# Performance work log

Measured on AMD Instinct MI355X. Metric: run time of the kernel, lower is better.

## Reference

```python
import jax, jax.numpy as jnp
import numpy as np

N = 100000
E = 1600000
IN = 256
H = 4
F = 64
NEG_SLOPE = 0.05


def setup_inputs() -> dict:
    key = jax.random.key(0)
    ks = jax.random.split(key, 8)
    feat = jax.random.normal(ks[0], (N, IN), dtype=jnp.float32)
    src = jax.random.randint(ks[1], (E,), 0, N, dtype=jnp.int64)
    dst = jax.random.randint(ks[2], (E,), 0, N, dtype=jnp.int64)
    W_fc = jax.random.normal(ks[3], (H * F, IN), dtype=jnp.float32) * (2.0 / np.sqrt(IN + H * F))
    attn_l = jax.random.normal(ks[4], (H, F), dtype=jnp.float32) * 0.1
    attn_r = jax.random.normal(ks[5], (H, F), dtype=jnp.float32) * 0.1
    W_res = jax.random.normal(ks[6], (H * F, IN), dtype=jnp.float32) * (2.0 / np.sqrt(IN + H * F))
    bias = jnp.zeros((H * F,), dtype=jnp.float32)
    return {"feat": feat, "src": src, "dst": dst, "W_fc": W_fc,
            "attn_l": attn_l, "attn_r": attn_r, "W_res": W_res, "bias": bias}


def _leaky_relu(x):
    return jnp.where(x > 0, x, NEG_SLOPE * x)


def reference(feat, src, dst, W_fc, attn_l, attn_r, W_res, bias):
    # project: [N, H, F]
    feat_src = (feat @ W_fc.T).reshape(N, H, F)
    # attention logits per node: el/er [N, H]
    el = jnp.einsum('nhf,hf->nh', feat_src, attn_l)
    er = jnp.einsum('nhf,hf->nh', feat_src, attn_r)
    # edge SDDMM (u_add_v) + leaky_relu: [E, H]
    e = _leaky_relu(el[src] + er[dst])
    # edge softmax grouped by destination node
    emax = jax.ops.segment_max(e, dst, num_segments=N)          # [N, H]
    emax = jnp.where(jnp.isfinite(emax), emax, 0.0)             # empty segments
    ex = jnp.exp(e - emax[dst])                                 # [E, H]
    esum = jax.ops.segment_sum(ex, dst, num_segments=N)         # [N, H]
    a = ex / jnp.maximum(esum[dst], 1e-20)                      # [E, H]
    # u_mul_e + sum aggregation (SpMM): [N, H, F]
    msgs = feat_src[src] * a[:, :, None]                        # [E, H, F]
    rst = jax.ops.segment_sum(msgs, dst, num_segments=N)
    # residual + bias
    rst = rst + (feat @ W_res.T).reshape(N, H, F)
    rst = rst + bias.reshape(1, H, F)
    return rst, a
```

## Files before the change

### kernel.cpp

```cpp
#include <hip/hip_runtime.h>

#define NNODES 100000
#define NEDGES 1600000
#define KDIM 256
#define CDIM 256
#define NHEAD 4
#define FDIM 64
#define NEG 0.05f

typedef short bf16x8 __attribute__((ext_vector_type(8)));
typedef float f32x4  __attribute__((ext_vector_type(4)));
typedef __attribute__((address_space(3))) void*       lds_vp;
typedef __attribute__((address_space(1))) const void* glb_cvp;

__device__ __forceinline__ unsigned short f2b(float x) {
    unsigned int u = __float_as_uint(x);
    return (unsigned short)((u + 0x7FFFu + ((u >> 16) & 1u)) >> 16);
}
__device__ __forceinline__ float b2f(unsigned short b) {
    return __uint_as_float(((unsigned int)b) << 16);
}
__device__ __forceinline__ float lrelu(float x) { return x > 0.f ? x : NEG * x; }

__device__ __forceinline__ unsigned int fmap(float f) {
    unsigned int u = __float_as_uint(f);
    return u ^ ((u >> 31) ? 0xFFFFFFFFu : 0x80000000u);
}
__device__ __forceinline__ float funmap(unsigned int u) {
    return __uint_as_float(u ^ ((u & 0x80000000u) ? 0x80000000u : 0xFFFFFFFFu));
}

__global__ __launch_bounds__(256) void cvt_feat(const float* __restrict__ in,
                                                unsigned short* __restrict__ out)
{
    int i = (blockIdx.x * 256 + threadIdx.x) * 4;
    float4 v = *(const float4*)(in + i);
    ushort4 o;
    o.x = f2b(v.x); o.y = f2b(v.y); o.z = f2b(v.z); o.w = f2b(v.w);
    *(ushort4*)(out + i) = o;
}

__global__ __launch_bounds__(256) void cvt_w(const float* __restrict__ Wfc,
                                             const float* __restrict__ Wres,
                                             unsigned short* __restrict__ out)
{
    int i = (blockIdx.x * 256 + threadIdx.x) * 4;
    float4 v = (i < 65536) ? *(const float4*)(Wfc + i)
                           : *(const float4*)(Wres + (i - 65536));
    ushort4 o;
    o.x = f2b(v.x); o.y = f2b(v.y); o.z = f2b(v.z); o.w = f2b(v.w);
    *(ushort4*)(out + i) = o;
}

__global__ __launch_bounds__(256) void gemm_mfma(
    const unsigned short* __restrict__ featb,
    const unsigned short* __restrict__ Wb,
    const float* __restrict__ bias,
    const float* __restrict__ attn_l, const float* __restrict__ attn_r,
    unsigned short* __restrict__ fsb,
    float* __restrict__ rst,
    float* __restrict__ el, float* __restrict__ er)
{
    const int b = blockIdx.x;
    const int grp = b >> 5, w32 = b & 31;
    const int bx = grp * 8 + (w32 & 7);
    const int ny = w32 >> 3;
    if (bx >= (NNODES + 127) / 128) return;

    __shared__ __align__(16) char smem[32768];
    char* sA = smem;
    char* sB = smem + 16384;

    const int tid = threadIdx.x;
    const int w = tid >> 6, l = tid & 63;
    const int wm = w & 1, wn = w >> 1;
    const int row0 = bx * 128;

    f32x4 acc[4][4];
#pragma unroll
    for (int tm = 0; tm < 4; ++tm)
#pragma unroll
        for (int tn = 0; tn < 4; ++tn) acc[tm][tn] = (f32x4)0.f;

    const int srow = tid >> 3;
    const int sslot = tid & 7;

    for (int k0 = 0; k0 < 256; k0 += 64) {
        if (k0) __syncthreads();
#pragma unroll
        for (int it = 0; it < 4; ++it) {
            int r = srow + it * 32;
            int gr = row0 + r; if (gr >= NNODES) gr = NNODES - 1;
            int kc = sslot ^ (r & 7);
            const unsigned short* g = featb + (size_t)gr * 256 + k0 + kc * 8;
            void* sp = sA + (it * 256 + w * 64) * 16;
            __builtin_amdgcn_global_load_lds((glb_cvp)g, (lds_vp)sp, 16, 0, 0);
        }
#pragma unroll
        for (int it = 0; it < 4; ++it) {
            int r = srow + it * 32;
            int kc = sslot ^ (r & 7);
            const unsigned short* g = Wb + (size_t)(ny * 128 + r) * 256 + k0 + kc * 8;
            void* sp = sB + (it * 256 + w * 64) * 16;
            __builtin_amdgcn_global_load_lds((glb_cvp)g, (lds_vp)sp, 16, 0, 0);
        }
        __syncthreads();

        const int quad = l >> 4;
#pragma unroll
        for (int kk = 0; kk < 2; ++kk) {
            const int kc = kk * 4 + quad;
            bf16x8 af[4], bq[4];
#pragma unroll
            for (int tm = 0; tm < 4; ++tm) {
                int m = wm * 64 + tm * 16 + (l & 15);
                af[tm] = *(const bf16x8*)(sA + m * 128 + ((kc ^ (m & 7)) * 16));
            }
#pragma unroll
            for (int tn = 0; tn < 4; ++tn) {
                int n = wn * 64 + tn * 16 + (l & 15);
                bq[tn] = *(const bf16x8*)(sB + n * 128 + ((kc ^ (n & 7)) * 16));
            }
#pragma unroll
            for (int tm = 0; tm < 4; ++tm)
#pragma unroll
                for (int tn = 0; tn < 4; ++tn)
                    acc[tm][tn] = __builtin_amdgcn_mfma_f32_16x16x32_bf16(
                        af[tm], bq[tn], acc[tm][tn], 0, 0, 0);
        }
    }

    const int quad = l >> 4, c15 = l & 15;
    if (ny < 2) {
#pragma unroll
        for (int tm = 0; tm < 4; ++tm) {
            int rb = row0 + wm * 64 + tm * 16 + quad * 4;
#pragma unroll
            for (int tn = 0; tn < 4; ++tn) {
                int cg = ny * 128 + wn * 64 + tn * 16 + c15;
#pragma unroll
                for (int reg = 0; reg < 4; ++reg) {
                    int r = rb + reg;
                    if (r < NNODES) fsb[(size_t)r * 256 + cg] = f2b(acc[tm][tn][reg]);
                }
            }
        }
        const int hh = ny * 2 + wn;
        float alv[4], arv[4];
#pragma unroll
        for (int tn = 0; tn < 4; ++tn) {
            alv[tn] = attn_l[hh * 64 + tn * 16 + c15];
            arv[tn] = attn_r[hh * 64 + tn * 16 + c15];
        }
#pragma unroll
        for (int tm = 0; tm < 4; ++tm) {
#pragma unroll
            for (int reg = 0; reg < 4; ++reg) {
                float pl = 0.f, pr = 0.f;
#pragma unroll
                for (int tn = 0; tn < 4; ++tn) {
                    float v = acc[tm][tn][reg];
                    pl = fmaf(v, alv[tn], pl);
                    pr = fmaf(v, arv[tn], pr);
                }
#pragma unroll
                for (int d = 1; d < 16; d <<= 1) {
                    pl += __shfl_xor(pl, d);
                    pr += __shfl_xor(pr, d);
                }
                if (c15 == 0) {
                    int r = row0 + wm * 64 + tm * 16 + quad * 4 + reg;
                    if (r < NNODES) {
                        el[r * NHEAD + hh] = pl;
                        er[r * NHEAD + hh] = pr;
                    }
                }
            }
        }
    } else {
#pragma unroll
        for (int tm = 0; tm < 4; ++tm) {
            int rb = row0 + wm * 64 + tm * 16 + quad * 4;
#pragma unroll
            for (int tn = 0; tn < 4; ++tn) {
                int co = (ny - 2) * 128 + wn * 64 + tn * 16 + c15;
                float b2 = bias[co];
#pragma unroll
                for (int reg = 0; reg < 4; ++reg) {
                    int r = rb + reg;
                    if (r < NNODES) rst[(size_t)r * 256 + co] = acc[tm][tn][reg] + b2;
                }
            }
        }
    }
}

__global__ __launch_bounds__(256) void gmax_kernel(const float* __restrict__ el,
                                                   unsigned int* __restrict__ gmax)
{
    int t = blockIdx.x * 256 + threadIdx.x;
    float4 mx = make_float4(-1e30f, -1e30f, -1e30f, -1e30f);
    for (int n = t; n < NNODES; n += 64 * 256) {
        float4 v = *(const float4*)(el + (size_t)n * 4);
        mx.x = fmaxf(mx.x, v.x); mx.y = fmaxf(mx.y, v.y);
        mx.z = fmaxf(mx.z, v.z); mx.w = fmaxf(mx.w, v.w);
    }
#pragma unroll
    for (int d = 32; d > 0; d >>= 1) {
        mx.x = fmaxf(mx.x, __shfl_xor(mx.x, d));
        mx.y = fmaxf(mx.y, __shfl_xor(mx.y, d));
        mx.z = fmaxf(mx.z, __shfl_xor(mx.z, d));
        mx.w = fmaxf(mx.w, __shfl_xor(mx.w, d));
    }
    if ((threadIdx.x & 63) == 0) {
        atomicMax(&gmax[0], fmap(mx.x));
        atomicMax(&gmax[1], fmap(mx.y));
        atomicMax(&gmax[2], fmap(mx.z));
        atomicMax(&gmax[3], fmap(mx.w));
    }
}

__global__ __launch_bounds__(256) void count_kernel(const int* __restrict__ dst,
                                                    int* __restrict__ cnt)
{
    int e = blockIdx.x * 256 + threadIdx.x;
    if (e < NEDGES) atomicAdd(&cnt[dst[e]], 1);
}

__global__ __launch_bounds__(256) void offset_kernel(const int* __restrict__ cnt,
                                                     int* __restrict__ off,
                                                     int* __restrict__ cursor,
                                                     int* __restrict__ total)
{
    int n = blockIdx.x * 256 + threadIdx.x;
    int lane = threadIdx.x & 63;
    int c = (n < NNODES) ? cnt[n] : 0;
    int incl = c;
#pragma unroll
    for (int d = 1; d < 64; d <<= 1) {
        int t = __shfl_up(incl, d);
        if (lane >= d) incl += t;
    }
    int wsum = __shfl(incl, 63);
    int base = 0;
    if (lane == 0) base = atomicAdd(total, wsum);
    base = __shfl(base, 0);
    if (n < NNODES) {
        int o = base + incl - c;
        off[n] = o;
        cursor[n] = o;
    }
}

__global__ __launch_bounds__(256) void scatter_kernel(const int* __restrict__ dst,
                                                      int* __restrict__ cursor,
                                                      int* __restrict__ perm)
{
    int e = blockIdx.x * 256 + threadIdx.x;
    if (e < NEDGES) {
        int p = atomicAdd(&cursor[dst[e]], 1);
        perm[p] = e;
    }
}

__global__ __launch_bounds__(256) void agg_kernel(
    const int* __restrict__ src, const int* __restrict__ perm,
    const int* __restrict__ off, const int* __restrict__ cnt,
    const float* __restrict__ el, const float* __restrict__ er,
    const unsigned int* __restrict__ gmax,
    const unsigned short* __restrict__ fsb,
    float* __restrict__ rst,
    float* __restrict__ a_out)
{
    const int tid = threadIdx.x;
    const int wv = tid >> 6, lane = tid & 63;
    const int n = blockIdx.x * 4 + wv;
    const int deg = cnt[n];
    if (deg == 0) return;
    const int o0 = off[n];

    __shared__ __align__(16) float a_sh[4][64][4];
    float* aw = &a_sh[wv][0][0];

    const float4 er4 = *(const float4*)(er + (size_t)n * NHEAD);
    const uint4 g4 = *(const uint4*)gmax;
    float4 M;
    M.x = lrelu(funmap(g4.x) + er4.x);
    M.y = lrelu(funmap(g4.y) + er4.y);
    M.z = lrelu(funmap(g4.z) + er4.z);
    M.w = lrelu(funmap(g4.w) + er4.w);

    float4 s = make_float4(0.f, 0.f, 0.f, 0.f);
    int s0_save = 0, e0_save = 0;
    float4 l0_save = make_float4(0.f, 0.f, 0.f, 0.f);

    for (int base = 0; base < deg; base += 64) {
        int i = base + lane;
        bool valid = i < deg;
        int e = perm[o0 + (valid ? i : deg - 1)];
        int sidx = src[e];
        float4 ev = *(const float4*)(el + (size_t)sidx * NHEAD);
        float4 l;
        l.x = lrelu(ev.x + er4.x); l.y = lrelu(ev.y + er4.y);
        l.z = lrelu(ev.z + er4.z); l.w = lrelu(ev.w + er4.w);
        if (base == 0) { s0_save = sidx; e0_save = e; l0_save = l; }
        s.x += valid ? __expf(l.x - M.x) : 0.f;
        s.y += valid ? __expf(l.y - M.y) : 0.f;
        s.z += valid ? __expf(l.z - M.z) : 0.f;
        s.w += valid ? __expf(l.w - M.w) : 0.f;
    }
#pragma unroll
    for (int d = 32; d > 0; d >>= 1) {
        s.x += __shfl_xor(s.x, d);
        s.y += __shfl_xor(s.y, d);
        s.z += __shfl_xor(s.z, d);
        s.w += __shfl_xor(s.w, d);
    }
    float4 inv;
    inv.x = 1.f / fmaxf(s.x, 1e-20f);
    inv.y = 1.f / fmaxf(s.y, 1e-20f);
    inv.z = 1.f / fmaxf(s.z, 1e-20f);
    inv.w = 1.f / fmaxf(s.w, 1e-20f);

    const int rsel = lane >> 5;
    const int c    = lane & 31;
    const int h2   = c >> 3;
    const unsigned int coff = (unsigned)c << 4;

    float acc[8];
#pragma unroll
    for (int k = 0; k < 8; ++k) acc[k] = 0.f;

    for (int base = 0; base < deg; base += 64) {
        int i = base + lane;
        bool valid = i < deg;
        int sidx, e; float4 l;
        if (base == 0) { sidx = s0_save; e = e0_save; l = l0_save; }
        else {
            e = perm[o0 + (valid ? i : deg - 1)];
            sidx = src[e];
            float4 ev = *(const float4*)(el + (size_t)sidx * NHEAD);
            l.x = lrelu(ev.x + er4.x); l.y = lrelu(ev.y + er4.y);
            l.z = lrelu(ev.z + er4.z); l.w = lrelu(ev.w + er4.w);
        }
        float4 a;
        a.x = valid ? __expf(l.x - M.x) * inv.x : 0.f;
        a.y = valid ? __expf(l.y - M.y) * inv.y : 0.f;
        a.z = valid ? __expf(l.z - M.z) * inv.z : 0.f;
        a.w = valid ? __expf(l.w - M.w) * inv.w : 0.f;
        *(float4*)(aw + (lane << 2)) = a;

        if (valid) *(float4*)(a_out + (size_t)e * NHEAD) = a;

        int nc = min(64, deg - base);
#pragma unroll 4
        for (int jj = 0; jj < nc; jj += 2) {
            int sjA = __builtin_amdgcn_readlane(sidx, jj);
            int sjB = __builtin_amdgcn_readlane(sidx, jj + 1);
            float av = aw[((jj + rsel) << 2) + h2];
            int sj = rsel ? sjB : sjA;
            unsigned int boff = ((unsigned)sj << 9) + coff;
            uint4 p = *(const uint4*)((const char*)fsb + boff);
            acc[0] = fmaf(av, __uint_as_float(p.x << 16),         acc[0]);
            acc[1] = fmaf(av, __uint_as_float(p.x & 0xffff0000u), acc[1]);
            acc[2] = fmaf(av, __uint_as_float(p.y << 16),         acc[2]);
            acc[3] = fmaf(av, __uint_as_float(p.y & 0xffff0000u), acc[3]);
            acc[4] = fmaf(av, __uint_as_float(p.z << 16),         acc[4]);
            acc[5] = fmaf(av, __uint_as_float(p.z & 0xffff0000u), acc[5]);
            acc[6] = fmaf(av, __uint_as_float(p.w << 16),         acc[6]);
            acc[7] = fmaf(av, __uint_as_float(p.w & 0xffff0000u), acc[7]);
        }
    }
#pragma unroll
    for (int k = 0; k < 8; ++k) acc[k] += __shfl_xor(acc[k], 32);
    float o0v = rsel ? acc[4] : acc[0];
    float o1v = rsel ? acc[5] : acc[1];
    float o2v = rsel ? acc[6] : acc[2];
    float o3v = rsel ? acc[7] : acc[3];
    size_t ro = (size_t)n * 256 + ((size_t)c << 3) + ((size_t)rsel << 2);
    float4 r = *(float4*)(rst + ro);
    r.x += o0v; r.y += o1v; r.z += o2v; r.w += o3v;
    *(float4*)(rst + ro) = r;
}

extern "C" void kernel_launch(void* const* d_in, const int* in_sizes, int n_in,
                              void* d_out, int out_size, void* d_ws, size_t ws_size,
                              hipStream_t stream) {
    const float* feat   = (const float*)d_in[0];
    const int*   src    = (const int*)d_in[1];
    const int*   dst    = (const int*)d_in[2];
    const float* Wfc    = (const float*)d_in[3];
    const float* attn_l = (const float*)d_in[4];
    const float* attn_r = (const float*)d_in[5];
    const float* Wres   = (const float*)d_in[6];
    const float* bias   = (const float*)d_in[7];

    float* rst   = (float*)d_out;
    float* a_out = (float*)d_out + (size_t)NNODES * CDIM;

    unsigned short* featb = (unsigned short*)d_ws;
    unsigned short* fsb   = featb + (size_t)NNODES * CDIM;
    unsigned short* Wb    = fsb + (size_t)NNODES * CDIM;
    float* el      = (float*)(Wb + 512 * 256);
    float* er      = el + (size_t)NNODES * NHEAD;
    unsigned int* gmax = (unsigned int*)(er + (size_t)NNODES * NHEAD);
    int* cnt    = (int*)(gmax + 4);
    int* off    = cnt + NNODES;
    int* cursor = off + NNODES;
    int* total  = cursor + NNODES;
    int* perm   = total + 4;

    hipMemsetAsync(cnt, 0, NNODES * sizeof(int), stream);
    hipMemsetAsync(total, 0, 4 * sizeof(int), stream);
    hipMemsetAsync(gmax, 0, 4 * sizeof(unsigned int), stream);

    cvt_feat<<<(NNODES * CDIM) / (256 * 4), 256, 0, stream>>>(feat, featb);
    cvt_w<<<(512 * 256) / (256 * 4), 256, 0, stream>>>(Wfc, Wres, Wb);

    gemm_mfma<<<3136, 256, 0, stream>>>(featb, Wb, bias, attn_l, attn_r,
                                        fsb, rst, el, er);

    gmax_kernel<<<64, 256, 0, stream>>>(el, gmax);

    count_kernel<<<(NEDGES + 255) / 256, 256, 0, stream>>>(dst, cnt);
    offset_kernel<<<(NNODES + 255) / 256, 256, 0, stream>>>(cnt, off, cursor, total);
    scatter_kernel<<<(NEDGES + 255) / 256, 256, 0, stream>>>(dst, cursor, perm);

    agg_kernel<<<NNODES / 4, 256, 0, stream>>>(src, perm, off, cnt, el, er, gmax,
                                               fsb, rst, a_out);
}
```

Measured before the change: 691.6 us.

## Fuse degree count into feature convert and pack src with edge permutation

The destination degree count moves into the bf16 feature-conversion kernel, removing one launch. The scatter step now writes (edge, src) pairs into a buffer that reuses the bf16 feature workspace, which is dead after the GEMM. This removes the dependent src[e] gather in both aggregation passes. The inner aggregation loop unroll grows from 4 to 8, and the change relies on the bf16 feature buffer being unused once the GEMM finishes.

```diff
diff --git a/kernel.cpp b/kernel.cpp
--- a/kernel.cpp
+++ b/kernel.cpp
@@ -30,14 +30,19 @@
     return __uint_as_float(u ^ ((u & 0x80000000u) ? 0x80000000u : 0xFFFFFFFFu));
 }
 
-__global__ __launch_bounds__(256) void cvt_feat(const float* __restrict__ in,
-                                                unsigned short* __restrict__ out)
+__global__ __launch_bounds__(256) void cvt_feat_count(
+    const float* __restrict__ in, unsigned short* __restrict__ out,
+    const int* __restrict__ dst, int* __restrict__ cnt)
 {
     int i = (blockIdx.x * 256 + threadIdx.x) * 4;
     float4 v = *(const float4*)(in + i);
     ushort4 o;
     o.x = f2b(v.x); o.y = f2b(v.y); o.z = f2b(v.z); o.w = f2b(v.w);
     *(ushort4*)(out + i) = o;
+    if (blockIdx.x < NEDGES / 256) {
+        int e = blockIdx.x * 256 + threadIdx.x;
+        atomicAdd(&cnt[dst[e]], 1);
+    }
 }
 
 __global__ __launch_bounds__(256) void cvt_w(const float* __restrict__ Wfc,
@@ -220,13 +225,6 @@
     }
 }
 
-__global__ __launch_bounds__(256) void count_kernel(const int* __restrict__ dst,
-                                                    int* __restrict__ cnt)
-{
-    int e = blockIdx.x * 256 + threadIdx.x;
-    if (e < NEDGES) atomicAdd(&cnt[dst[e]], 1);
-}
-
 __global__ __launch_bounds__(256) void offset_kernel(const int* __restrict__ cnt,
                                                      int* __restrict__ off,
                                                      int* __restrict__ cursor,
@@ -253,18 +251,20 @@
 }
 
 __global__ __launch_bounds__(256) void scatter_kernel(const int* __restrict__ dst,
+                                                      const int* __restrict__ src,
                                                       int* __restrict__ cursor,
-                                                      int* __restrict__ perm)
+                                                      int2* __restrict__ eperm)
 {
     int e = blockIdx.x * 256 + threadIdx.x;
     if (e < NEDGES) {
+        int s = src[e];
         int p = atomicAdd(&cursor[dst[e]], 1);
-        perm[p] = e;
+        eperm[p] = make_int2(e, s);
     }
 }
 
 __global__ __launch_bounds__(256) void agg_kernel(
-    const int* __restrict__ src, const int* __restrict__ perm,
+    const int2* __restrict__ eperm,
     const int* __restrict__ off, const int* __restrict__ cnt,
     const float* __restrict__ el, const float* __restrict__ er,
     const unsigned int* __restrict__ gmax,
@@ -297,13 +297,13 @@
     for (int base = 0; base < deg; base += 64) {
         int i = base + lane;
         bool valid = i < deg;
-        int e = perm[o0 + (valid ? i : deg - 1)];
-        int sidx = src[e];
+        int2 es = eperm[o0 + (valid ? i : deg - 1)];
+        int sidx = es.y;
         float4 ev = *(const float4*)(el + (size_t)sidx * NHEAD);
         float4 l;
         l.x = lrelu(ev.x + er4.x); l.y = lrelu(ev.y + er4.y);
         l.z = lrelu(ev.z + er4.z); l.w = lrelu(ev.w + er4.w);
-        if (base == 0) { s0_save = sidx; e0_save = e; l0_save = l; }
+        if (base == 0) { s0_save = sidx; e0_save = es.x; l0_save = l; }
         s.x += valid ? __expf(l.x - M.x) : 0.f;
         s.y += valid ? __expf(l.y - M.y) : 0.f;
         s.z += valid ? __expf(l.z - M.z) : 0.f;
@@ -337,8 +337,8 @@
         int sidx, e; float4 l;
         if (base == 0) { sidx = s0_save; e = e0_save; l = l0_save; }
         else {
-            e = perm[o0 + (valid ? i : deg - 1)];
-            sidx = src[e];
+            int2 es = eperm[o0 + (valid ? i : deg - 1)];
+            e = es.x; sidx = es.y;
             float4 ev = *(const float4*)(el + (size_t)sidx * NHEAD);
             l.x = lrelu(ev.x + er4.x); l.y = lrelu(ev.y + er4.y);
             l.z = lrelu(ev.z + er4.z); l.w = lrelu(ev.w + er4.w);
@@ -353,7 +353,7 @@
         if (valid) *(float4*)(a_out + (size_t)e * NHEAD) = a;
 
         int nc = min(64, deg - base);
-#pragma unroll 4
+#pragma unroll 8
         for (int jj = 0; jj < nc; jj += 2) {
             int sjA = __builtin_amdgcn_readlane(sidx, jj);
             int sjB = __builtin_amdgcn_readlane(sidx, jj + 1);
@@ -408,13 +408,14 @@
     int* off    = cnt + NNODES;
     int* cursor = off + NNODES;
     int* total  = cursor + NNODES;
-    int* perm   = total + 4;
+    int2* eperm = (int2*)featb;
 
     hipMemsetAsync(cnt, 0, NNODES * sizeof(int), stream);
     hipMemsetAsync(total, 0, 4 * sizeof(int), stream);
     hipMemsetAsync(gmax, 0, 4 * sizeof(unsigned int), stream);
 
-    cvt_feat<<<(NNODES * CDIM) / (256 * 4), 256, 0, stream>>>(feat, featb);
+    cvt_feat_count<<<(NNODES * CDIM) / (256 * 4), 256, 0, stream>>>(feat, featb,
+                                                                    dst, cnt);
     cvt_w<<<(512 * 256) / (256 * 4), 256, 0, stream>>>(Wfc, Wres, Wb);
 
     gemm_mfma<<<3136, 256, 0, stream>>>(featb, Wb, bias, attn_l, attn_r,
@@ -422,10 +423,10 @@
 
     gmax_kernel<<<64, 256, 0, stream>>>(el, gmax);
 
-    count_kernel<<<(NEDGES + 255) / 256, 256, 0, stream>>>(dst, cnt);
     offset_kernel<<<(NNODES + 255) / 256, 256, 0, stream>>>(cnt, off, cursor, total);
-    scatter_kernel<<<(NEDGES + 255) / 256, 256, 0, stream>>>(dst, cursor, perm);
-
-    agg_kernel<<<NNODES / 4, 256, 0, stream>>>(src, perm, off, cnt, el, er, gmax,
+    scatter_kernel<<<(NEDGES + 255) / 256, 256, 0, stream>>>(dst, src, cursor,
+                                                             eperm);
+
+    agg_kernel<<<NNODES / 4, 256, 0, stream>>>(eperm, off, cnt, el, er, gmax,
                                                fsb, rst, a_out);
 }
```

Measured after the change: 625.6 us. 1.11x faster.
